# Optimization experiments

Measured on AMD Instinct MI355X. Metric: run time of the kernel, lower is better.

## Reference

```python
import jax, jax.numpy as jnp
import numpy as np

B, T, S, E, H = 64, 512, 512, 512, 512


def setup_inputs() -> dict:
    key = jax.random.key(0)
    ks = jax.random.split(key, 10)
    g = lambda k, shape: jax.random.normal(k, shape, jnp.float32) * 0.05
    return {
        "input_embeddings": g(ks[0], (B, T, E)),
        "encoder_outputs": g(ks[1], (B, S, H)),
        "encoder_masks": jnp.zeros((B, S), dtype=bool),  # True = masked position
        "W_ih": g(ks[2], (3 * H, E)),
        "W_hh": g(ks[3], (3 * H, H)),
        "b_ih": g(ks[4], (3 * H,)),
        "b_hh": g(ks[5], (3 * H,)),
        "W_attn_out": g(ks[6], (H, 2 * H)),
        "b_attn_out": g(ks[7], (H,)),
        "W_dense": g(ks[8], (H, H)),
        "b_dense": g(ks[9], (H,)),
    }


def _gru(x, W_ih, W_hh, b_ih, b_hh):
    # PyTorch GRU math, single layer, h0 = 0. x: [B,T,E] -> ([B,T,H], [B,H])
    Hn = W_hh.shape[1]
    xi = jnp.einsum('bte,ge->btg', x, W_ih) + b_ih  # precompute input proj [B,T,3H]

    def step(h, xi_t):
        hh = h @ W_hh.T + b_hh
        xr, xz, xn = jnp.split(xi_t, 3, axis=-1)
        hr, hz, hn = jnp.split(hh, 3, axis=-1)
        r = jax.nn.sigmoid(xr + hr)
        z = jax.nn.sigmoid(xz + hz)
        n = jnp.tanh(xn + r * hn)
        h_new = (1.0 - z) * n + z * h
        return h_new, h_new

    h0 = jnp.zeros((x.shape[0], Hn), x.dtype)
    h_last, hs = jax.lax.scan(step, h0, jnp.swapaxes(xi, 0, 1))
    return jnp.swapaxes(hs, 0, 1), h_last


def reference(input_embeddings, encoder_outputs, encoder_masks,
              W_ih, W_hh, b_ih, b_hh, W_attn_out, b_attn_out, W_dense, b_dense):
    # GRU output at each step == its hidden state; attention does not feed back,
    # so the per-step torch loop is equivalent to: scan the GRU, then batched attention.
    dec_out, h_last = _gru(input_embeddings, W_ih, W_hh, b_ih, b_hh)  # [B,T,H]
    # SeqAttention: dot-product scores, mask-fill -inf, softmax, mix, tanh(Linear(2H->H))
    scores = jnp.einsum('bth,bsh->bts', dec_out, encoder_outputs)
    scores = jnp.where(encoder_masks[:, None, :], -jnp.inf, scores)
    attn = jax.nn.softmax(scores, axis=-1)
    mix = jnp.einsum('bts,bsh->bth', attn, encoder_outputs)
    combined = jnp.concatenate([mix, dec_out], axis=-1)  # [B,T,2H]
    out = jnp.tanh(combined @ W_attn_out.T + b_attn_out)
    # attention_dense: Linear(H, H)
    out = out @ W_dense.T + b_dense  # [B,T,H]
    return out, h_last[None]  # hidden_states: [num_layers=1, B, H]
```

## Files before the change

kernel.cpp:

```cpp
#include <hip/hip_runtime.h>

typedef __attribute__((ext_vector_type(8))) short bf16x8;
typedef __attribute__((ext_vector_type(4))) float f32x4;

#define MFMA16(a, b, c) __builtin_amdgcn_mfma_f32_16x16x32_bf16((a), (b), (c), 0, 0, 0)

__device__ __forceinline__ unsigned short f2bf(float f) {
    unsigned int u = __builtin_bit_cast(unsigned int, f);
    u = (u + 0x7fffu + ((u >> 16) & 1u)) >> 16;
    return (unsigned short)u;
}
__device__ __forceinline__ float bf2f(unsigned short s) {
    unsigned int u = ((unsigned int)s) << 16;
    return __builtin_bit_cast(float, u);
}
__device__ __forceinline__ bf16x8 pack8(float4 a, float4 b) {
    bf16x8 v;
    v[0] = (short)f2bf(a.x); v[1] = (short)f2bf(a.y);
    v[2] = (short)f2bf(a.z); v[3] = (short)f2bf(a.w);
    v[4] = (short)f2bf(b.x); v[5] = (short)f2bf(b.y);
    v[6] = (short)f2bf(b.z); v[7] = (short)f2bf(b.w);
    return v;
}
__device__ __forceinline__ float sigmoidf_(float x) { return 1.0f / (1.0f + __expf(-x)); }
__device__ __forceinline__ float tanhf_(float x) { return 2.0f / (1.0f + __expf(-2.0f * x)) - 1.0f; }

__global__ void k_cvt(const float* __restrict__ s, unsigned short* __restrict__ d, int n8) {
    int i = blockIdx.x * blockDim.x + threadIdx.x;
    int stride = gridDim.x * blockDim.x;
    for (; i < n8; i += stride) {
        const float4* sp = (const float4*)(s + (size_t)i * 8);
        float4 a = sp[0], b = sp[1];
        *(bf16x8*)(d + (size_t)i * 8) = pack8(a, b);
    }
}

__global__ void k_transpose(const unsigned short* __restrict__ src, unsigned short* __restrict__ dst) {
    __shared__ unsigned short tile[64][66];
    const int b = blockIdx.x, s0 = blockIdx.y * 64, h0 = blockIdx.z * 64;
    const int tx = threadIdx.x, ty = threadIdx.y;
    for (int r = ty; r < 64; r += 4)
        tile[r][tx] = src[((size_t)(b * 512) + (s0 + r)) * 512 + h0 + tx];
    __syncthreads();
    for (int r = ty; r < 64; r += 4)
        dst[((size_t)(b * 512) + (h0 + r)) * 512 + s0 + tx] = tile[tx][r];
}

__global__ __launch_bounds__(256) void k_gemm_xi(
    const float* __restrict__ emb, const float* __restrict__ W_ih,
    const float* __restrict__ b_ih, unsigned short* __restrict__ xi) {
    __shared__ unsigned short Asub[2][4096];
    __shared__ unsigned short Bsub[2][4096];
    const int tid = threadIdx.x;
    const int wv = tid >> 6, l = tid & 63, lr = l & 15, lu = l >> 4;
    const int wm = wv >> 1, wn = wv & 1;
    const int row0 = blockIdx.x * 128, col0 = blockIdx.y * 128;

    f32x4 acc[4][4];
#pragma unroll
    for (int mt = 0; mt < 4; ++mt)
#pragma unroll
        for (int nt = 0; nt < 4; ++nt) acc[mt][nt] = (f32x4){0.f, 0.f, 0.f, 0.f};

    bf16x8 sA[2], sB[2];
    auto ldstage = [&](int ks) {
#pragma unroll
        for (int i = 0; i < 2; ++i) {
            int chunk = i * 256 + tid;
            int row = chunk >> 2;
            int ce = (chunk & 3) * 8;
            const float* pa = emb + (size_t)(row0 + row) * 512 + ks * 32 + ce;
            sA[i] = pack8(((const float4*)pa)[0], ((const float4*)pa)[1]);
            const float* pb = W_ih + (size_t)(col0 + row) * 512 + ks * 32 + ce;
            sB[i] = pack8(((const float4*)pb)[0], ((const float4*)pb)[1]);
        }
    };
    auto wrstage = [&](int buf) {
#pragma unroll
        for (int i = 0; i < 2; ++i) {
            int chunk = i * 256 + tid;
            int idx = (chunk & 3) * 1024 + (chunk >> 2) * 8;
            *(bf16x8*)(&Asub[buf][idx]) = sA[i];
            *(bf16x8*)(&Bsub[buf][idx]) = sB[i];
        }
    };
    ldstage(0);
    wrstage(0);
    __syncthreads();
#pragma unroll 1
    for (int ks = 0; ks < 16; ++ks) {
        const int cb = ks & 1;
        if (ks < 15) ldstage(ks + 1);
        bf16x8 af[4];
#pragma unroll
        for (int mt = 0; mt < 4; ++mt)
            af[mt] = *(const bf16x8*)(&Asub[cb][lu * 1024 + (wm * 64 + mt * 16 + lr) * 8]);
#pragma unroll
        for (int nt = 0; nt < 4; ++nt) {
            bf16x8 bb = *(const bf16x8*)(&Bsub[cb][lu * 1024 + (wn * 64 + nt * 16 + lr) * 8]);
#pragma unroll
            for (int mt = 0; mt < 4; ++mt) acc[mt][nt] = MFMA16(af[mt], bb, acc[mt][nt]);
        }
        if (ks < 15) wrstage(cb ^ 1);
        __syncthreads();
    }
#pragma unroll
    for (int nt = 0; nt < 4; ++nt) {
        const int col = col0 + wn * 64 + nt * 16 + lr;
        const float bias = b_ih[col];
#pragma unroll
        for (int mt = 0; mt < 4; ++mt)
#pragma unroll
            for (int j = 0; j < 4; ++j) {
                const int row = row0 + wm * 64 + mt * 16 + lu * 4 + j;
                xi[(size_t)row * 1536 + col] = f2bf(acc[mt][nt][j] + bias);
            }
    }
}

__global__ __attribute__((amdgpu_flat_work_group_size(512, 512), amdgpu_waves_per_eu(2, 2)))
void k_scan(
    const float* __restrict__ W_hh, const float* __restrict__ b_hh,
    const unsigned short* __restrict__ xi,
    unsigned short* __restrict__ dec, float* __restrict__ hlast,
    unsigned short* hb,
    unsigned int* flags) {
    __shared__ unsigned short hlds[16 * 512];
    __shared__ unsigned short hstage[16 * 128];
    const int tid = threadIdx.x;
    const int w = tid >> 6, l = tid & 63, lr = l & 15, lu = l >> 4;
    const int g = blockIdx.x & 3;
    const int q = blockIdx.x >> 2;
    const int bg0 = g * 16;
    const int hcol = q * 128 + w * 16 + lr;
    unsigned short* hb_g = hb + g * 16384;
    unsigned int* flag_g = flags + g * 2048;

    bf16x8 wf[3][16];
#pragma unroll
    for (int g3 = 0; g3 < 3; ++g3) {
        const float* wr = W_hh + (size_t)(g3 * 512 + hcol) * 512;
#pragma unroll
        for (int kt = 0; kt < 16; ++kt) {
            const float* p = wr + kt * 32 + lu * 8;
            wf[g3][kt] = pack8(*(const float4*)p, *(const float4*)(p + 4));
        }
    }
    float bh[3];
#pragma unroll
    for (int g3 = 0; g3 < 3; ++g3) bh[g3] = b_hh[g3 * 512 + hcol];

    unsigned short xv[12];
#pragma unroll
    for (int g3 = 0; g3 < 3; ++g3)
#pragma unroll
        for (int j = 0; j < 4; ++j)
            xv[g3 * 4 + j] = xi[((size_t)(bg0 + lu * 4 + j) * 512 + 0) * 1536 + g3 * 512 + hcol];

    float hloc[4] = {0.f, 0.f, 0.f, 0.f};

#pragma clang loop unroll(disable)
    for (int t = 0; t < 512; ++t) {
        if (t > 0) {
            if (tid < 4) {
                while (__hip_atomic_load(&flag_g[(t - 1) * 4 + tid],
                                         __ATOMIC_RELAXED, __HIP_MEMORY_SCOPE_AGENT) == 0u)
                    __builtin_amdgcn_s_sleep(1);
            }
            __syncthreads();
        }
        {
            unsigned long long* src = (unsigned long long*)(hb_g + (t & 1) * 8192);
#pragma unroll
            for (int i = 0; i < 4; ++i) {
                int c = i * 512 + tid;
                unsigned long long v = __hip_atomic_load(src + c, __ATOMIC_RELAXED, __HIP_MEMORY_SCOPE_AGENT);
                int row = c >> 7;
                int colb = (c & 127) * 8;
                *(unsigned long long*)((char*)hlds + row * 1024 + (colb ^ ((row & 7) << 4))) = v;
            }
        }
        __syncthreads();
        f32x4 acc0 = (f32x4){0.f, 0.f, 0.f, 0.f};
        f32x4 acc1 = (f32x4){0.f, 0.f, 0.f, 0.f};
        f32x4 acc2 = (f32x4){0.f, 0.f, 0.f, 0.f};
#pragma unroll
        for (int kt = 0; kt < 16; ++kt) {
            bf16x8 a = *(const bf16x8*)((char*)hlds + lr * 1024 + ((kt * 64 + lu * 16) ^ ((lr & 7) << 4)));
            acc0 = MFMA16(a, wf[0][kt], acc0);
            acc1 = MFMA16(a, wf[1][kt], acc1);
            acc2 = MFMA16(a, wf[2][kt], acc2);
        }
#pragma unroll
        for (int j = 0; j < 4; ++j) {
            float xr = bf2f(xv[0 * 4 + j]);
            float xz = bf2f(xv[1 * 4 + j]);
            float xn = bf2f(xv[2 * 4 + j]);
            float rr = sigmoidf_(xr + acc0[j] + bh[0]);
            float zz = sigmoidf_(xz + acc1[j] + bh[1]);
            float nn = tanhf_(xn + rr * (acc2[j] + bh[2]));
            float hv = (1.f - zz) * nn + zz * hloc[j];
            hloc[j] = hv;
            int row = lu * 4 + j;
            int colb = (w * 32 + lr * 2) ^ ((row & 7) << 4);
            *(unsigned short*)((char*)hstage + row * 256 + colb) = f2bf(hv);
        }
        if (t < 511) {
#pragma unroll
            for (int g3 = 0; g3 < 3; ++g3)
#pragma unroll
                for (int j = 0; j < 4; ++j)
                    xv[g3 * 4 + j] = xi[((size_t)(bg0 + lu * 4 + j) * 512 + (t + 1)) * 1536 + g3 * 512 + hcol];
        }
        __syncthreads();
        {
            int r = tid >> 5, c8 = tid & 31;
            unsigned long long v = *(unsigned long long*)((char*)hstage + r * 256 + ((c8 * 8) ^ ((r & 7) << 4)));
            if (t < 511)
                __hip_atomic_store(
                    (unsigned long long*)(hb_g + ((t + 1) & 1) * 8192 + r * 512 + q * 128) + c8, v,
                    __ATOMIC_RELAXED, __HIP_MEMORY_SCOPE_AGENT);
            *((unsigned long long*)(dec + ((size_t)(bg0 + r) * 512 + t) * 512 + q * 128) + c8) = v;
        }
        __syncthreads();
        if (t < 511 && tid == 0)
            __hip_atomic_store(&flag_g[t * 4 + q], 1u, __ATOMIC_RELEASE, __HIP_MEMORY_SCOPE_AGENT);
    }
#pragma unroll
    for (int j = 0; j < 4; ++j)
        hlast[(size_t)(bg0 + lu * 4 + j) * 512 + hcol] = hloc[j];
}

__global__ __launch_bounds__(256) void k_attn(
    const unsigned short* __restrict__ dec, const unsigned short* __restrict__ enc,
    const unsigned short* __restrict__ encT, const unsigned char* __restrict__ masks,
    unsigned short* __restrict__ mix) {
    __shared__ char Pt[65536];
    __shared__ float red[64][4];
    const int tid = threadIdx.x, w = tid >> 6, l = tid & 63, lr = l & 15, lu = l >> 4;
    const int b = blockIdx.x >> 3, t0 = (blockIdx.x & 7) << 6;
    const size_t encBase = (size_t)b * 512 * 512;

    {
        const char* src = (const char*)(dec + (size_t)(b * 512 + t0) * 512);
#pragma unroll
        for (int i = 0; i < 16; ++i) {
            int chunk = i * 256 + tid;
            int row = chunk >> 6;
            int colb = (chunk & 63) * 16;
            uint4 v = *(const uint4*)(src + (size_t)row * 1024 + colb);
            *(uint4*)(Pt + row * 1024 + (colb ^ ((row & 7) << 4))) = v;
        }
    }
    __syncthreads();

    f32x4 acc[4][8];
#pragma unroll
    for (int mt = 0; mt < 4; ++mt)
#pragma unroll
        for (int nt = 0; nt < 8; ++nt) acc[mt][nt] = (f32x4){0.f, 0.f, 0.f, 0.f};

#pragma unroll 2
    for (int kt = 0; kt < 16; ++kt) {
        bf16x8 af[4];
#pragma unroll
        for (int mt = 0; mt < 4; ++mt)
            af[mt] = *(const bf16x8*)(Pt + (mt * 16 + lr) * 1024 + ((kt * 64 + lu * 16) ^ ((lr & 7) << 4)));
#pragma unroll
        for (int nt = 0; nt < 8; ++nt) {
            bf16x8 bb = *(const bf16x8*)(enc + encBase + (size_t)(w * 128 + nt * 16 + lr) * 512 + kt * 32 + lu * 8);
#pragma unroll
            for (int mt = 0; mt < 4; ++mt) acc[mt][nt] = MFMA16(af[mt], bb, acc[mt][nt]);
        }
    }
#pragma unroll
    for (int nt = 0; nt < 8; ++nt) {
        if (masks[b * 512 + w * 128 + nt * 16 + lr]) {
#pragma unroll
            for (int mt = 0; mt < 4; ++mt)
#pragma unroll
                for (int j = 0; j < 4; ++j) acc[mt][nt][j] = -3.0e38f;
        }
    }
    float rmax[4][4], rinv[4][4];
#pragma unroll
    for (int mt = 0; mt < 4; ++mt)
#pragma unroll
        for (int j = 0; j < 4; ++j) {
            float m = acc[mt][0][j];
#pragma unroll
            for (int nt = 1; nt < 8; ++nt) m = fmaxf(m, acc[mt][nt][j]);
            m = fmaxf(m, __shfl_xor(m, 1));
            m = fmaxf(m, __shfl_xor(m, 2));
            m = fmaxf(m, __shfl_xor(m, 4));
            m = fmaxf(m, __shfl_xor(m, 8));
            if (lr == 0) red[mt * 16 + lu * 4 + j][w] = m;
        }
    __syncthreads();
#pragma unroll
    for (int mt = 0; mt < 4; ++mt)
#pragma unroll
        for (int j = 0; j < 4; ++j) {
            float4 v = *(const float4*)(&red[mt * 16 + lu * 4 + j][0]);
            rmax[mt][j] = fmaxf(fmaxf(v.x, v.y), fmaxf(v.z, v.w));
        }
    __syncthreads();
#pragma unroll
    for (int mt = 0; mt < 4; ++mt)
#pragma unroll
        for (int j = 0; j < 4; ++j) {
            float s = 0.f;
#pragma unroll
            for (int nt = 0; nt < 8; ++nt) {
                float e = __expf(acc[mt][nt][j] - rmax[mt][j]);
                acc[mt][nt][j] = e;
                s += e;
            }
            s += __shfl_xor(s, 1);
            s += __shfl_xor(s, 2);
            s += __shfl_xor(s, 4);
            s += __shfl_xor(s, 8);
            if (lr == 0) red[mt * 16 + lu * 4 + j][w] = s;
        }
    __syncthreads();
#pragma unroll
    for (int mt = 0; mt < 4; ++mt)
#pragma unroll
        for (int j = 0; j < 4; ++j) {
            float4 v = *(const float4*)(&red[mt * 16 + lu * 4 + j][0]);
            rinv[mt][j] = 1.f / (v.x + v.y + v.z + v.w);
        }
#pragma unroll
    for (int mt = 0; mt < 4; ++mt)
#pragma unroll
        for (int nt = 0; nt < 8; ++nt)
#pragma unroll
            for (int j = 0; j < 4; ++j) {
                int row = mt * 16 + lu * 4 + j;
                int colb = (w * 128 + nt * 16 + lr) * 2;
                *(unsigned short*)(Pt + row * 1024 + (colb ^ ((row & 7) << 4))) =
                    f2bf(acc[mt][nt][j] * rinv[mt][j]);
            }
    __syncthreads();
#pragma unroll
    for (int mt = 0; mt < 4; ++mt)
#pragma unroll
        for (int nt = 0; nt < 8; ++nt) acc[mt][nt] = (f32x4){0.f, 0.f, 0.f, 0.f};
#pragma unroll 2
    for (int kt = 0; kt < 16; ++kt) {
        bf16x8 af[4];
#pragma unroll
        for (int mt = 0; mt < 4; ++mt)
            af[mt] = *(const bf16x8*)(Pt + (mt * 16 + lr) * 1024 + ((kt * 64 + lu * 16) ^ ((lr & 7) << 4)));
#pragma unroll
        for (int nt = 0; nt < 8; ++nt) {
            bf16x8 bb = *(const bf16x8*)(encT + encBase + (size_t)(w * 128 + nt * 16 + lr) * 512 + kt * 32 + lu * 8);
#pragma unroll
            for (int mt = 0; mt < 4; ++mt) acc[mt][nt] = MFMA16(af[mt], bb, acc[mt][nt]);
        }
    }
#pragma unroll
    for (int mt = 0; mt < 4; ++mt)
#pragma unroll
        for (int nt = 0; nt < 8; ++nt)
#pragma unroll
            for (int j = 0; j < 4; ++j) {
                int row = mt * 16 + lu * 4 + j, col = w * 128 + nt * 16 + lr;
                mix[(size_t)(b * 512 + t0 + row) * 512 + col] = f2bf(acc[mt][nt][j]);
            }
}

__global__ __launch_bounds__(256) void k_out(
    const unsigned short* __restrict__ mix, const unsigned short* __restrict__ dec,
    const unsigned short* __restrict__ Wa, const float* __restrict__ ba,
    const unsigned short* __restrict__ Wd, const float* __restrict__ bd,
    float* __restrict__ out) {
    __shared__ char At[65536];
    const int tid = threadIdx.x, w = tid >> 6, l = tid & 63, lr = l & 15, lu = l >> 4;
    const int b = blockIdx.x >> 3, t0 = (blockIdx.x & 7) << 6;

    f32x4 acc[4][8];
#pragma unroll
    for (int mt = 0; mt < 4; ++mt)
#pragma unroll
        for (int nt = 0; nt < 8; ++nt) acc[mt][nt] = (f32x4){0.f, 0.f, 0.f, 0.f};

#pragma unroll 1
    for (int half = 0; half < 2; ++half) {
        const unsigned short* srcp = half ? dec : mix;
        const char* src = (const char*)(srcp + (size_t)(b * 512 + t0) * 512);
#pragma unroll
        for (int i = 0; i < 16; ++i) {
            int chunk = i * 256 + tid;
            int row = chunk >> 6;
            int colb = (chunk & 63) * 16;
            uint4 v = *(const uint4*)(src + (size_t)row * 1024 + colb);
            *(uint4*)(At + row * 1024 + (colb ^ ((row & 7) << 4))) = v;
        }
        __syncthreads();
#pragma unroll 2
        for (int kt = 0; kt < 16; ++kt) {
            bf16x8 af[4];
#pragma unroll
            for (int mt = 0; mt < 4; ++mt)
                af[mt] = *(const bf16x8*)(At + (mt * 16 + lr) * 1024 + ((kt * 64 + lu * 16) ^ ((lr & 7) << 4)));
#pragma unroll
            for (int nt = 0; nt < 8; ++nt) {
                bf16x8 bb = *(const bf16x8*)(Wa + (size_t)(w * 128 + nt * 16 + lr) * 1024 + half * 512 + kt * 32 + lu * 8);
#pragma unroll
                for (int mt = 0; mt < 4; ++mt) acc[mt][nt] = MFMA16(af[mt], bb, acc[mt][nt]);
            }
        }
        __syncthreads();
    }
    float bav[8];
#pragma unroll
    for (int nt = 0; nt < 8; ++nt) bav[nt] = ba[w * 128 + nt * 16 + lr];
#pragma unroll
    for (int mt = 0; mt < 4; ++mt)
#pragma unroll
        for (int nt = 0; nt < 8; ++nt)
#pragma unroll
            for (int j = 0; j < 4; ++j) {
                float v = tanhf_(acc[mt][nt][j] + bav[nt]);
                int row = mt * 16 + lu * 4 + j;
                int colb = (w * 128 + nt * 16 + lr) * 2;
                *(unsigned short*)(At + row * 1024 + (colb ^ ((row & 7) << 4))) = f2bf(v);
            }
    __syncthreads();
#pragma unroll
    for (int mt = 0; mt < 4; ++mt)
#pragma unroll
        for (int nt = 0; nt < 8; ++nt) acc[mt][nt] = (f32x4){0.f, 0.f, 0.f, 0.f};
#pragma unroll 2
    for (int kt = 0; kt < 16; ++kt) {
        bf16x8 af[4];
#pragma unroll
        for (int mt = 0; mt < 4; ++mt)
            af[mt] = *(const bf16x8*)(At + (mt * 16 + lr) * 1024 + ((kt * 64 + lu * 16) ^ ((lr & 7) << 4)));
#pragma unroll
        for (int nt = 0; nt < 8; ++nt) {
            bf16x8 bb = *(const bf16x8*)(Wd + (size_t)(w * 128 + nt * 16 + lr) * 512 + kt * 32 + lu * 8);
#pragma unroll
            for (int mt = 0; mt < 4; ++mt) acc[mt][nt] = MFMA16(af[mt], bb, acc[mt][nt]);
        }
    }
#pragma unroll
    for (int nt = 0; nt < 8; ++nt) {
        const int col = w * 128 + nt * 16 + lr;
        const float bdv = bd[col];
#pragma unroll
        for (int mt = 0; mt < 4; ++mt)
#pragma unroll
            for (int j = 0; j < 4; ++j) {
                int row = mt * 16 + lu * 4 + j;
                out[(size_t)(b * 512 + t0 + row) * 512 + col] = acc[mt][nt][j] + bdv;
            }
    }
}

extern "C" void kernel_launch(void* const* d_in, const int* in_sizes, int n_in,
                              void* d_out, int out_size, void* d_ws, size_t ws_size,
                              hipStream_t stream) {
    const float* emb = (const float*)d_in[0];
    const float* enc_f = (const float*)d_in[1];
    const unsigned char* masks = (const unsigned char*)d_in[2];
    const float* W_ih = (const float*)d_in[3];
    const float* W_hh = (const float*)d_in[4];
    const float* b_ih = (const float*)d_in[5];
    const float* b_hh = (const float*)d_in[6];
    const float* W_a = (const float*)d_in[7];
    const float* b_a = (const float*)d_in[8];
    const float* W_d = (const float*)d_in[9];
    const float* b_d = (const float*)d_in[10];
    float* out = (float*)d_out;

    char* ws = (char*)d_ws;
    unsigned short* xi    = (unsigned short*)(ws + 0);
    unsigned short* encb  = (unsigned short*)(ws + 100663296);
    unsigned short* encT  = (unsigned short*)(ws + 134217728);
    unsigned short* decb  = (unsigned short*)(ws + 167772160);
    unsigned short* mixb  = (unsigned short*)(ws + 201326592);
    unsigned short* Wab   = (unsigned short*)(ws + 234881024);
    unsigned short* Wdb   = (unsigned short*)(ws + 235929600);
    unsigned short* hb    = (unsigned short*)(ws + 236453888);
    unsigned int*   flags = (unsigned int*)(ws + 236584960);

    hipMemsetAsync(ws + 236453888, 0, 163840, stream);

    k_cvt<<<1024, 256, 0, stream>>>(enc_f, encb, 16777216 / 8);
    k_cvt<<<256, 256, 0, stream>>>(W_a, Wab, 524288 / 8);
    k_cvt<<<128, 256, 0, stream>>>(W_d, Wdb, 262144 / 8);
    k_transpose<<<dim3(64, 8, 8), dim3(64, 4), 0, stream>>>(encb, encT);
    k_gemm_xi<<<dim3(256, 12), 256, 0, stream>>>(emb, W_ih, b_ih, xi);
    k_scan<<<16, 512, 0, stream>>>(W_hh, b_hh, xi, decb, out + 16777216, hb, flags);
    k_attn<<<512, 256, 0, stream>>>(decb, encb, encT, masks, mixb);
    k_out<<<512, 256, 0, stream>>>(mixb, decb, Wab, b_a, Wdb, b_d, out);
}
```

Baseline: 3.153 ms.

## Split GRU scan across 32 blocks with split-K MFMA and LDS reduction

The recurrent scan now runs on 32 workgroups of 1024 threads instead of 16 of 512. Each group owns 64 hidden columns, and four wave groups split the K dimension of the W_hh matmul, then reduce their partial sums through shared memory. This cuts per-wave serial MFMA depth and register weight footprint on the latency-bound recurrence. In exchange it adds an LDS reduction, an extra barrier per step, and more cross-block flag polling per timestep (8 producers instead of 4).

Measured after the change: 2.785 ms. 1.13x faster.

```diff
diff --git a/kernel.cpp b/kernel.cpp
--- a/kernel.cpp
+++ b/kernel.cpp
@@ -2,6 +2,7 @@
 
 typedef __attribute__((ext_vector_type(8))) short bf16x8;
 typedef __attribute__((ext_vector_type(4))) float f32x4;
+typedef unsigned long long u64;
 
 #define MFMA16(a, b, c) __builtin_amdgcn_mfma_f32_16x16x32_bf16((a), (b), (c), 0, 0, 0)
 
@@ -118,117 +119,139 @@
     }
 }
 
-__global__ __attribute__((amdgpu_flat_work_group_size(512, 512), amdgpu_waves_per_eu(2, 2)))
-void k_scan(
+__global__ __launch_bounds__(1024) void k_scan(
     const float* __restrict__ W_hh, const float* __restrict__ b_hh,
     const unsigned short* __restrict__ xi,
     unsigned short* __restrict__ dec, float* __restrict__ hlast,
     unsigned short* hb,
     unsigned int* flags) {
     __shared__ unsigned short hlds[16 * 512];
-    __shared__ unsigned short hstage[16 * 128];
+    __shared__ f32x4 gacc[3][4][4][64];
+    __shared__ unsigned short hstage[16 * 64];
     const int tid = threadIdx.x;
     const int w = tid >> 6, l = tid & 63, lr = l & 15, lu = l >> 4;
+    const int ct = w & 3, ks = w >> 2;
     const int g = blockIdx.x & 3;
     const int q = blockIdx.x >> 2;
     const int bg0 = g * 16;
-    const int hcol = q * 128 + w * 16 + lr;
+    const int col = q * 64 + ct * 16 + lr;
     unsigned short* hb_g = hb + g * 16384;
-    unsigned int* flag_g = flags + g * 2048;
-
-    bf16x8 wf[3][16];
+    unsigned int* flag_g = flags + g * 4096;
+
+    bf16x8 wf[3][4];
 #pragma unroll
     for (int g3 = 0; g3 < 3; ++g3) {
-        const float* wr = W_hh + (size_t)(g3 * 512 + hcol) * 512;
-#pragma unroll
-        for (int kt = 0; kt < 16; ++kt) {
-            const float* p = wr + kt * 32 + lu * 8;
-            wf[g3][kt] = pack8(*(const float4*)p, *(const float4*)(p + 4));
-        }
-    }
-    float bh[3];
-#pragma unroll
-    for (int g3 = 0; g3 < 3; ++g3) bh[g3] = b_hh[g3 * 512 + hcol];
-
+        const float* wr = W_hh + (size_t)(g3 * 512 + col) * 512;
+#pragma unroll
+        for (int kk = 0; kk < 4; ++kk) {
+            const float* p = wr + (ks * 4 + kk) * 32 + lu * 8;
+            wf[g3][kk] = pack8(*(const float4*)p, *(const float4*)(p + 4));
+        }
+    }
+
+    float bh[3] = {0.f, 0.f, 0.f};
     unsigned short xv[12];
-#pragma unroll
-    for (int g3 = 0; g3 < 3; ++g3)
-#pragma unroll
-        for (int j = 0; j < 4; ++j)
-            xv[g3 * 4 + j] = xi[((size_t)(bg0 + lu * 4 + j) * 512 + 0) * 1536 + g3 * 512 + hcol];
-
     float hloc[4] = {0.f, 0.f, 0.f, 0.f};
+    if (w < 4) {
+#pragma unroll
+        for (int g3 = 0; g3 < 3; ++g3) bh[g3] = b_hh[g3 * 512 + col];
+#pragma unroll
+        for (int g3 = 0; g3 < 3; ++g3)
+#pragma unroll
+            for (int j = 0; j < 4; ++j)
+                xv[g3 * 4 + j] = xi[((size_t)(bg0 + lu * 4 + j) * 512) * 1536 + g3 * 512 + col];
+    }
 
 #pragma clang loop unroll(disable)
     for (int t = 0; t < 512; ++t) {
         if (t > 0) {
-            if (tid < 4) {
-                while (__hip_atomic_load(&flag_g[(t - 1) * 4 + tid],
+            if (tid < 8) {
+                while (__hip_atomic_load(&flag_g[(t - 1) * 8 + tid],
                                          __ATOMIC_RELAXED, __HIP_MEMORY_SCOPE_AGENT) == 0u)
                     __builtin_amdgcn_s_sleep(1);
             }
             __syncthreads();
         }
         {
-            unsigned long long* src = (unsigned long long*)(hb_g + (t & 1) * 8192);
-#pragma unroll
-            for (int i = 0; i < 4; ++i) {
-                int c = i * 512 + tid;
-                unsigned long long v = __hip_atomic_load(src + c, __ATOMIC_RELAXED, __HIP_MEMORY_SCOPE_AGENT);
+            const u64* src = (const u64*)(hb_g + (t & 1) * 8192);
+#pragma unroll
+            for (int i = 0; i < 2; ++i) {
+                int c = i * 1024 + tid;
+                u64 v = __hip_atomic_load(src + c, __ATOMIC_RELAXED, __HIP_MEMORY_SCOPE_AGENT);
                 int row = c >> 7;
                 int colb = (c & 127) * 8;
-                *(unsigned long long*)((char*)hlds + row * 1024 + (colb ^ ((row & 7) << 4))) = v;
-            }
-        }
-        __syncthreads();
-        f32x4 acc0 = (f32x4){0.f, 0.f, 0.f, 0.f};
-        f32x4 acc1 = (f32x4){0.f, 0.f, 0.f, 0.f};
-        f32x4 acc2 = (f32x4){0.f, 0.f, 0.f, 0.f};
-#pragma unroll
-        for (int kt = 0; kt < 16; ++kt) {
+                *(u64*)((char*)hlds + row * 1024 + (colb ^ ((row & 7) << 4))) = v;
+            }
+        }
+        __syncthreads();
+        f32x4 a0 = (f32x4){0.f, 0.f, 0.f, 0.f};
+        f32x4 a1 = (f32x4){0.f, 0.f, 0.f, 0.f};
+        f32x4 a2 = (f32x4){0.f, 0.f, 0.f, 0.f};
+#pragma unroll
+        for (int kk = 0; kk < 4; ++kk) {
+            const int kt = ks * 4 + kk;
             bf16x8 a = *(const bf16x8*)((char*)hlds + lr * 1024 + ((kt * 64 + lu * 16) ^ ((lr & 7) << 4)));
-            acc0 = MFMA16(a, wf[0][kt], acc0);
-            acc1 = MFMA16(a, wf[1][kt], acc1);
-            acc2 = MFMA16(a, wf[2][kt], acc2);
-        }
-#pragma unroll
-        for (int j = 0; j < 4; ++j) {
-            float xr = bf2f(xv[0 * 4 + j]);
-            float xz = bf2f(xv[1 * 4 + j]);
-            float xn = bf2f(xv[2 * 4 + j]);
-            float rr = sigmoidf_(xr + acc0[j] + bh[0]);
-            float zz = sigmoidf_(xz + acc1[j] + bh[1]);
-            float nn = tanhf_(xn + rr * (acc2[j] + bh[2]));
-            float hv = (1.f - zz) * nn + zz * hloc[j];
-            hloc[j] = hv;
-            int row = lu * 4 + j;
-            int colb = (w * 32 + lr * 2) ^ ((row & 7) << 4);
-            *(unsigned short*)((char*)hstage + row * 256 + colb) = f2bf(hv);
-        }
-        if (t < 511) {
-#pragma unroll
-            for (int g3 = 0; g3 < 3; ++g3)
-#pragma unroll
-                for (int j = 0; j < 4; ++j)
-                    xv[g3 * 4 + j] = xi[((size_t)(bg0 + lu * 4 + j) * 512 + (t + 1)) * 1536 + g3 * 512 + hcol];
-        }
-        __syncthreads();
-        {
-            int r = tid >> 5, c8 = tid & 31;
-            unsigned long long v = *(unsigned long long*)((char*)hstage + r * 256 + ((c8 * 8) ^ ((r & 7) << 4)));
+            a0 = MFMA16(a, wf[0][kk], a0);
+            a1 = MFMA16(a, wf[1][kk], a1);
+            a2 = MFMA16(a, wf[2][kk], a2);
+        }
+        gacc[0][ks][ct][l] = a0;
+        gacc[1][ks][ct][l] = a1;
+        gacc[2][ks][ct][l] = a2;
+        __syncthreads();
+        if (w < 4) {
+            f32x4 s0 = gacc[0][0][ct][l];
+            f32x4 s1 = gacc[1][0][ct][l];
+            f32x4 s2 = gacc[2][0][ct][l];
+#pragma unroll
+            for (int k2 = 1; k2 < 4; ++k2) {
+                s0 += gacc[0][k2][ct][l];
+                s1 += gacc[1][k2][ct][l];
+                s2 += gacc[2][k2][ct][l];
+            }
+#pragma unroll
+            for (int j = 0; j < 4; ++j) {
+                float xr = bf2f(xv[0 * 4 + j]);
+                float xz = bf2f(xv[1 * 4 + j]);
+                float xn = bf2f(xv[2 * 4 + j]);
+                float rr = sigmoidf_(xr + s0[j] + bh[0]);
+                float zz = sigmoidf_(xz + s1[j] + bh[1]);
+                float nn = tanhf_(xn + rr * (s2[j] + bh[2]));
+                float hv = (1.f - zz) * nn + zz * hloc[j];
+                hloc[j] = hv;
+                int batch = lu * 4 + j;
+                int cw = ct * 16 + lr;
+                hstage[batch * 64 + (cw ^ ((batch & 7) << 3))] = f2bf(hv);
+            }
+            if (t < 511) {
+#pragma unroll
+                for (int g3 = 0; g3 < 3; ++g3)
+#pragma unroll
+                    for (int j = 0; j < 4; ++j)
+                        xv[g3 * 4 + j] =
+                            xi[((size_t)(bg0 + lu * 4 + j) * 512 + (t + 1)) * 1536 + g3 * 512 + col];
+            }
+        }
+        __syncthreads();
+        if (w >= 4 && w < 8) {
+            int i = tid - 256;
+            int batch = i >> 4, w8 = i & 15;
+            u64 v = ((const u64*)hstage)[batch * 16 + (w8 ^ ((batch & 7) << 1))];
             if (t < 511)
                 __hip_atomic_store(
-                    (unsigned long long*)(hb_g + ((t + 1) & 1) * 8192 + r * 512 + q * 128) + c8, v,
+                    (u64*)(hb_g + ((t + 1) & 1) * 8192 + batch * 512 + q * 64) + w8, v,
                     __ATOMIC_RELAXED, __HIP_MEMORY_SCOPE_AGENT);
-            *((unsigned long long*)(dec + ((size_t)(bg0 + r) * 512 + t) * 512 + q * 128) + c8) = v;
+            *((u64*)(dec + ((size_t)(bg0 + batch) * 512 + t) * 512 + q * 64) + w8) = v;
         }
         __syncthreads();
         if (t < 511 && tid == 0)
-            __hip_atomic_store(&flag_g[t * 4 + q], 1u, __ATOMIC_RELEASE, __HIP_MEMORY_SCOPE_AGENT);
-    }
-#pragma unroll
-    for (int j = 0; j < 4; ++j)
-        hlast[(size_t)(bg0 + lu * 4 + j) * 512 + hcol] = hloc[j];
+            __hip_atomic_store(&flag_g[t * 8 + q], 1u, __ATOMIC_RELEASE, __HIP_MEMORY_SCOPE_AGENT);
+    }
+    if (w < 4) {
+#pragma unroll
+        for (int j = 0; j < 4; ++j)
+            hlast[(size_t)(bg0 + lu * 4 + j) * 512 + col] = hloc[j];
+    }
 }
 
 __global__ __launch_bounds__(256) void k_attn(
@@ -486,14 +509,14 @@
     unsigned short* hb    = (unsigned short*)(ws + 236453888);
     unsigned int*   flags = (unsigned int*)(ws + 236584960);
 
-    hipMemsetAsync(ws + 236453888, 0, 163840, stream);
+    hipMemsetAsync(ws + 236453888, 0, 196608, stream);
 
     k_cvt<<<1024, 256, 0, stream>>>(enc_f, encb, 16777216 / 8);
     k_cvt<<<256, 256, 0, stream>>>(W_a, Wab, 524288 / 8);
     k_cvt<<<128, 256, 0, stream>>>(W_d, Wdb, 262144 / 8);
     k_transpose<<<dim3(64, 8, 8), dim3(64, 4), 0, stream>>>(encb, encT);
     k_gemm_xi<<<dim3(256, 12), 256, 0, stream>>>(emb, W_ih, b_ih, xi);
-    k_scan<<<16, 512, 0, stream>>>(W_hh, b_hh, xi, decb, out + 16777216, hb, flags);
+    k_scan<<<32, 1024, 0, stream>>>(W_hh, b_hh, xi, decb, out + 16777216, hb, flags);
     k_attn<<<512, 256, 0, stream>>>(decb, encb, encT, masks, mixb);
     k_out<<<512, 256, 0, stream>>>(mixb, decb, Wab, b_a, Wdb, b_d, out);
 }
```
